# Kernel tuning notes

Measured on AMD Instinct MI355X. Metric: run time of the kernel, lower is better.

## Reference

```python
import jax, jax.numpy as jnp
import numpy as np

D = 128
NM = 1043
ND = 2166
EM = 300000
ED = 600000


def _gcn(x, src, dst, w, W, b):
    # symmetric-normalized weighted GCN conv: out = A_norm @ (x W^T) + b
    n = x.shape[0]
    deg = jax.ops.segment_sum(w, dst, num_segments=n)
    dinv = jnp.where(deg > 0, 1.0 / jnp.sqrt(deg), 0.0)
    norm = dinv[src] * w * dinv[dst]          # [E]
    h = x @ W.T                               # [n, D]
    return jax.ops.segment_sum(h[src] * norm[:, None], dst, num_segments=n) + b


def _encoder(x, edge, w, W1, b1, W2, b2):
    src, dst = edge[0], edge[1]
    x1 = jax.nn.relu(_gcn(x, src, dst, w, W1, b1))
    x2 = jax.nn.relu(_gcn(x1, src, dst, w, W2, b2))
    return x1, x2


def _layer_view_att(x, fc1_W, fc1_b, fc2_W, fc2_b):
    # x: [C, D, N]; channel attention over views/layers (LayerViewAttention)
    a = x.mean(axis=(1, 2))                            # global avg pool -> [C]
    a = jax.nn.relu(a @ fc1_W.T + fc1_b)
    a = jax.nn.sigmoid(a @ fc2_W.T + fc2_b)
    return jax.nn.relu(x * a[:, None, None])


def _fcn(x, W1, b1, W2, b2):
    # Fcn fusion: Linear -> ReLU -> Linear -> ReLU
    h = jax.nn.relu(x @ W1.T + b1)
    return jax.nn.relu(h @ W2.T + b2)


def setup_inputs():
    key = jax.random.key(0)
    ks = iter(jax.random.split(key, 64))

    def nrm(shape, s=0.05):
        return jax.random.normal(next(ks), shape, jnp.float32) * s

    inp = {}
    inp["mirna_x"] = jax.random.normal(next(ks), (NM, D), jnp.float32)
    inp["drug_x"] = jax.random.normal(next(ks), (ND, D), jnp.float32)
    for pre, n, e in [("m1", NM, EM), ("m2", NM, EM), ("d1", ND, ED), ("d2", ND, ED)]:
        inp[pre + "_edge"] = jax.random.randint(next(ks), (2, e), 0, n, jnp.int32)
        inp[pre + "_w"] = jax.random.uniform(next(ks), (e,), jnp.float32)
        inp[pre + "_W1"] = nrm((D, D))
        inp[pre + "_b1"] = jnp.zeros((D,), jnp.float32)
        inp[pre + "_W2"] = nrm((D, D))
        inp[pre + "_b2"] = jnp.zeros((D,), jnp.float32)
    inp["m_fc1_W"] = nrm((4, 4)); inp["m_fc1_b"] = jnp.zeros((4,), jnp.float32)
    inp["m_fc2_W"] = nrm((4, 4)); inp["m_fc2_b"] = jnp.zeros((4,), jnp.float32)
    inp["d_fc1_W"] = nrm((2, 2)); inp["d_fc1_b"] = jnp.zeros((2,), jnp.float32)
    inp["d_fc2_W"] = nrm((2, 2)); inp["d_fc2_b"] = jnp.zeros((2,), jnp.float32)
    inp["m_fus_W1"] = nrm((2 * D, 4 * D)); inp["m_fus_b1"] = jnp.zeros((2 * D,), jnp.float32)
    inp["m_fus_W2"] = nrm((D, 2 * D));     inp["m_fus_b2"] = jnp.zeros((D,), jnp.float32)
    inp["d_fus_W1"] = nrm((2 * D, 2 * D)); inp["d_fus_b1"] = jnp.zeros((2 * D,), jnp.float32)
    inp["d_fus_W2"] = nrm((D, 2 * D));     inp["d_fus_b2"] = jnp.zeros((D,), jnp.float32)
    return inp


def reference(mirna_x, drug_x,
              m1_edge, m1_w, m1_W1, m1_b1, m1_W2, m1_b2,
              m2_edge, m2_w, m2_W1, m2_b1, m2_W2, m2_b2,
              d1_edge, d1_w, d1_W1, d1_b1, d1_W2, d1_b2,
              d2_edge, d2_w, d2_W1, d2_b1, d2_W2, d2_b2,
              m_fc1_W, m_fc1_b, m_fc2_W, m_fc2_b,
              d_fc1_W, d_fc1_b, d_fc2_W, d_fc2_b,
              m_fus_W1, m_fus_b1, m_fus_W2, m_fus_b2,
              d_fus_W1, d_fus_b1, d_fus_W2, d_fus_b2):
    # miRNA: 2 views x 2 layers -> 4 channels
    m1a, m1b = _encoder(mirna_x, m1_edge, m1_w, m1_W1, m1_b1, m1_W2, m1_b2)
    m2a, m2b = _encoder(mirna_x, m2_edge, m2_w, m2_W1, m2_b1, m2_W2, m2_b2)
    mx = jnp.stack([m1a, m1b, m2a, m2b], axis=0).transpose(0, 2, 1)   # [4, D, NM]
    mx = _layer_view_att(mx, m_fc1_W, m_fc1_b, m_fc2_W, m_fc2_b)
    m_out = _fcn(mx.transpose(2, 0, 1).reshape(NM, 4 * D),
                 m_fus_W1, m_fus_b1, m_fus_W2, m_fus_b2)             # [NM, D]
    # drug: views summed per layer -> 2 channels
    d1a, d1b = _encoder(drug_x, d1_edge, d1_w, d1_W1, d1_b1, d1_W2, d1_b2)
    d2a, d2b = _encoder(drug_x, d2_edge, d2_w, d2_W1, d2_b1, d2_W2, d2_b2)
    dx = jnp.stack([d1a + d2a, d1b + d2b], axis=0).transpose(0, 2, 1)  # [2, D, ND]
    dx = _layer_view_att(dx, d_fc1_W, d_fc1_b, d_fc2_W, d_fc2_b)
    d_out = _fcn(dx.transpose(2, 0, 1).reshape(ND, 2 * D),
                 d_fus_W1, d_fus_b1, d_fus_W2, d_fus_b2)             # [ND, D]
    return jnp.concatenate([m_out, d_out], axis=0)                   # [NM+ND, D]
```

## Files before the change

kernel.cpp:

```cpp
#include <hip/hip_runtime.h>
#include <math.h>

#define D128 128
#define NM_ 1043
#define ND_ 2166
#define EM_ 300000
#define ED_ 600000
#define NBH 64
#define NMAX 2176
#define NTOT 6418
#define ETOT 1800000

struct ViewArgs {
    const int* edge[4];
    const float* w[4];
    int n[4], E[4];
    int cumn[5];
    int cumE[5];
    int rpo[4];
};

struct BiasArr { const float* b[4]; };

__global__ __launch_bounds__(1024) void hist_b(ViewArgs va, int* __restrict__ pcnt,
                                               float* __restrict__ pdeg) {
    __shared__ int lc[NMAX];
    __shared__ float ld[NMAX];
    const int view = blockIdx.x >> 6, vb = blockIdx.x & 63;
    const int n = va.n[view], E = va.E[view];
    const int* edge = va.edge[view];
    const float* w = va.w[view];
    for (int i = threadIdx.x; i < n; i += 1024) { lc[i] = 0; ld[i] = 0.f; }
    __syncthreads();
    const int per = (E + NBH - 1) / NBH;
    const int b = vb * per, e = min(E, b + per);
    for (int i = b + threadIdx.x; i < e; i += 1024) {
        int dst = edge[E + i];
        atomicAdd(&lc[dst], 1);
        atomicAdd(&ld[dst], w[i]);
    }
    __syncthreads();
    int* pc = pcnt + (size_t)NBH * va.cumn[view] + (size_t)vb * n;
    float* pd = pdeg + (size_t)NBH * va.cumn[view] + (size_t)vb * n;
    for (int i = threadIdx.x; i < n; i += 1024) { pc[i] = lc[i]; pd[i] = ld[i]; }
}

__global__ void colred_b(ViewArgs va, const int* __restrict__ pcnt,
                         const float* __restrict__ pdeg, int* __restrict__ cnt,
                         float* __restrict__ dinv) {
    int i = blockIdx.x * 256 + threadIdx.x;
    if (i >= NTOT) return;
    int view = 0;
    while (view < 3 && i >= va.cumn[view + 1]) ++view;
    const int il = i - va.cumn[view], n = va.n[view];
    const int* pc = pcnt + (size_t)NBH * va.cumn[view];
    const float* pd = pdeg + (size_t)NBH * va.cumn[view];
    int c = 0;
    float dg = 0.f;
    for (int b = 0; b < NBH; ++b) {
        c += pc[(size_t)b * n + il];
        dg += pd[(size_t)b * n + il];
    }
    cnt[i] = c;
    dinv[i] = dg > 0.f ? 1.0f / sqrtf(dg) : 0.f;
}

__global__ void scan_b(ViewArgs va, const int* __restrict__ cnt, int* __restrict__ rowptr) {
    __shared__ int wsum[4];
    const int view = blockIdx.x;
    const int n = va.n[view];
    const int* c = cnt + va.cumn[view];
    int* rp = rowptr + va.rpo[view];
    const int tid = threadIdx.x;
    const int per = (n + 255) / 256;
    const int b0 = tid * per, e0 = min(n, b0 + per);
    int s = 0;
    for (int i = b0; i < e0; ++i) s += c[i];
    const int lane = tid & 63, wid = tid >> 6;
    int sc = s;
    for (int off = 1; off < 64; off <<= 1) {
        int t = __shfl_up(sc, off);
        if (lane >= off) sc += t;
    }
    if (lane == 63) wsum[wid] = sc;
    __syncthreads();
    int wbase = 0;
    for (int wv = 0; wv < wid; ++wv) wbase += wsum[wv];
    int run = wbase + sc - s;
    if (tid == 0) rp[0] = 0;
    for (int i = b0; i < e0; ++i) {
        run += c[i];
        rp[i + 1] = run;
    }
}

__global__ void cum_b(ViewArgs va, const int* __restrict__ pcnt,
                      const int* __restrict__ rowptr, int* __restrict__ cum) {
    int i = blockIdx.x * 256 + threadIdx.x;
    if (i >= NTOT) return;
    int view = 0;
    while (view < 3 && i >= va.cumn[view + 1]) ++view;
    const int il = i - va.cumn[view], n = va.n[view];
    const int* pc = pcnt + (size_t)NBH * va.cumn[view];
    int* cm = cum + (size_t)NBH * va.cumn[view];
    int run = rowptr[va.rpo[view] + il];
    for (int b = 0; b < NBH; ++b) {
        cm[(size_t)b * n + il] = run;
        run += pc[(size_t)b * n + il];
    }
}

__global__ __launch_bounds__(1024) void fill2_b(ViewArgs va, const float* __restrict__ dinv,
                                                const int* __restrict__ cum,
                                                int2* __restrict__ spair) {
    __shared__ int lc[NMAX];
    const int view = blockIdx.x >> 6, vb = blockIdx.x & 63;
    const int n = va.n[view], E = va.E[view];
    const int* edge = va.edge[view];
    const float* w = va.w[view];
    const int* cm = cum + (size_t)NBH * va.cumn[view] + (size_t)vb * n;
    const float* dv = dinv + va.cumn[view];
    int2* sp = spair + va.cumE[view];
    for (int i = threadIdx.x; i < n; i += 1024) lc[i] = cm[i];
    __syncthreads();
    const int per = (E + NBH - 1) / NBH;
    const int b = vb * per, e = min(E, b + per);
    for (int i = b + threadIdx.x; i < e; i += 1024) {
        int src = edge[i];
        int dst = edge[E + i];
        int pos = atomicAdd(&lc[dst], 1);
        float nrm = dv[src] * w[i] * dv[dst];
        sp[pos] = make_int2(src, __float_as_int(nrm));
    }
}

__global__ __launch_bounds__(128) void agg_b(ViewArgs va, const int2* __restrict__ spair,
                                             const int* __restrict__ rowptr,
                                             const float* __restrict__ h, BiasArr ba,
                                             float* __restrict__ outbuf) {
    const int nf = blockIdx.x;
    int view = 0;
    while (view < 3 && nf >= va.cumn[view + 1]) ++view;
    const int ln = nf - va.cumn[view];
    const int* rp = rowptr + va.rpo[view];
    const int beg = rp[ln], end = rp[ln + 1];
    const int2* sp = spair + va.cumE[view];
    const float* hb = h + (size_t)va.cumn[view] * D128;
    const int tid = threadIdx.x;
    float a0 = 0.f, a1 = 0.f, a2 = 0.f, a3 = 0.f;
    int i = beg;
    for (; i + 4 <= end; i += 4) {
        int2 p0 = sp[i], p1 = sp[i + 1], p2 = sp[i + 2], p3 = sp[i + 3];
        a0 = fmaf(__int_as_float(p0.y), hb[(size_t)p0.x * D128 + tid], a0);
        a1 = fmaf(__int_as_float(p1.y), hb[(size_t)p1.x * D128 + tid], a1);
        a2 = fmaf(__int_as_float(p2.y), hb[(size_t)p2.x * D128 + tid], a2);
        a3 = fmaf(__int_as_float(p3.y), hb[(size_t)p3.x * D128 + tid], a3);
    }
    for (; i < end; ++i)
        a0 = fmaf(__int_as_float(sp[i].y), hb[(size_t)sp[i].x * D128 + tid], a0);
    float v = (a0 + a1) + (a2 + a3);
    outbuf[(size_t)nf * D128 + tid] = fmaxf(v + ba.b[view][tid], 0.f);
}

struct GSeg {
    const float* A;
    const float* W;
    const float* bias;
    float* C;
    int M, N, K, rowblks, blk0, relu;
};
struct GArgs { GSeg s[4]; int nseg; };

__global__ __launch_bounds__(256) void gemm_b(GArgs ga) {
    __shared__ float xs[32 * 64];
    __shared__ float wsm[128 * 64];
    int si = 0;
    while (si + 1 < ga.nseg && (int)blockIdx.x >= ga.s[si + 1].blk0) ++si;
    const GSeg S = ga.s[si];
    const int lb = blockIdx.x - S.blk0;
    const int rb = lb % S.rowblks, cb = lb / S.rowblks;
    const int row0 = rb * 32, col0 = cb * 128;
    const int tid = threadIdx.x;
    const int r0 = (tid >> 5) << 2;
    const int c0 = tid & 31;
    const int csw = (c0 & 7) << 2;
    float acc[4][4] = {};
    for (int kc = 0; kc < S.K; kc += 64) {
#pragma unroll
        for (int it = 0; it < 2; ++it) {
            int idx = tid + it * 256;
            int r = idx >> 4, k4 = (idx & 15) << 2;
            int gr = row0 + r;
            if (gr > S.M - 1) gr = S.M - 1;
            *(float4*)(xs + r * 64 + k4) =
                *(const float4*)(S.A + (size_t)gr * S.K + kc + k4);
        }
#pragma unroll
        for (int it = 0; it < 8; ++it) {
            int idx = tid + it * 256;
            int c = idx >> 4, k4 = (idx & 15) << 2;
            *(float4*)(wsm + c * 64 + (k4 ^ ((c & 7) << 2))) =
                *(const float4*)(S.W + (size_t)(col0 + c) * S.K + kc + k4);
        }
        __syncthreads();
#pragma unroll
        for (int k4 = 0; k4 < 64; k4 += 4) {
            float4 a0 = *(const float4*)(xs + (r0 + 0) * 64 + k4);
            float4 a1 = *(const float4*)(xs + (r0 + 1) * 64 + k4);
            float4 a2 = *(const float4*)(xs + (r0 + 2) * 64 + k4);
            float4 a3 = *(const float4*)(xs + (r0 + 3) * 64 + k4);
            const int sk = k4 ^ csw;
            float4 w0 = *(const float4*)(wsm + (c0 + 0) * 64 + sk);
            float4 w1 = *(const float4*)(wsm + (c0 + 32) * 64 + sk);
            float4 w2 = *(const float4*)(wsm + (c0 + 64) * 64 + sk);
            float4 w3 = *(const float4*)(wsm + (c0 + 96) * 64 + sk);
#define FMA4(i, av)                                                   \
            acc[i][0] = fmaf(av.x, w0.x, acc[i][0]); acc[i][0] = fmaf(av.y, w0.y, acc[i][0]); \
            acc[i][0] = fmaf(av.z, w0.z, acc[i][0]); acc[i][0] = fmaf(av.w, w0.w, acc[i][0]); \
            acc[i][1] = fmaf(av.x, w1.x, acc[i][1]); acc[i][1] = fmaf(av.y, w1.y, acc[i][1]); \
            acc[i][1] = fmaf(av.z, w1.z, acc[i][1]); acc[i][1] = fmaf(av.w, w1.w, acc[i][1]); \
            acc[i][2] = fmaf(av.x, w2.x, acc[i][2]); acc[i][2] = fmaf(av.y, w2.y, acc[i][2]); \
            acc[i][2] = fmaf(av.z, w2.z, acc[i][2]); acc[i][2] = fmaf(av.w, w2.w, acc[i][2]); \
            acc[i][3] = fmaf(av.x, w3.x, acc[i][3]); acc[i][3] = fmaf(av.y, w3.y, acc[i][3]); \
            acc[i][3] = fmaf(av.z, w3.z, acc[i][3]); acc[i][3] = fmaf(av.w, w3.w, acc[i][3]);
            FMA4(0, a0) FMA4(1, a1) FMA4(2, a2) FMA4(3, a3)
#undef FMA4
        }
        __syncthreads();
    }
#pragma unroll
    for (int i = 0; i < 4; ++i) {
        int gr = row0 + r0 + i;
        if (gr < S.M) {
#pragma unroll
            for (int j = 0; j < 4; ++j) {
                int gc = col0 + c0 + 32 * j;
                float v = acc[i][j];
                if (S.bias) v += S.bias[gc];
                if (S.relu) v = fmaxf(v, 0.f);
                S.C[(size_t)gr * S.N + gc] = v;
            }
        }
    }
}

struct SumArgs {
    const float* p[8];
    int cnt[8];
};

__global__ __launch_bounds__(256) void sum8_kernel(SumArgs args, float* __restrict__ sums) {
    __shared__ float red[256];
    const int ch = blockIdx.y;
    const float* x = args.p[ch];
    const int count = args.cnt[ch];
    float s = 0.f;
    for (int i = blockIdx.x * 256 + threadIdx.x; i < count; i += gridDim.x * 256) s += x[i];
    red[threadIdx.x] = s;
    __syncthreads();
    for (int off = 128; off > 0; off >>= 1) {
        if (threadIdx.x < off) red[threadIdx.x] += red[threadIdx.x + off];
        __syncthreads();
    }
    if (threadIdx.x == 0) atomicAdd(&sums[ch], red[0]);
}

__global__ void att_kernel(const float* __restrict__ sums,
                           const float* __restrict__ mW1, const float* __restrict__ mb1,
                           const float* __restrict__ mW2, const float* __restrict__ mb2,
                           const float* __restrict__ dW1, const float* __restrict__ db1,
                           const float* __restrict__ dW2, const float* __restrict__ db2,
                           float* __restrict__ scales) {
    if (threadIdx.x != 0 || blockIdx.x != 0) return;
    float mean[4], a[4];
    const float invM = 1.0f / (128.f * (float)NM_);
    for (int c = 0; c < 4; ++c) mean[c] = sums[c] * invM;
    for (int i = 0; i < 4; ++i) {
        float v = mb1[i];
        for (int j = 0; j < 4; ++j) v += mW1[i * 4 + j] * mean[j];
        a[i] = fmaxf(v, 0.f);
    }
    for (int c = 0; c < 4; ++c) {
        float v = mb2[c];
        for (int j = 0; j < 4; ++j) v += mW2[c * 4 + j] * a[j];
        scales[c] = 1.f / (1.f + expf(-v));
    }
    const float invD = 1.0f / (128.f * (float)ND_);
    float md[2] = {(sums[4] + sums[6]) * invD, (sums[5] + sums[7]) * invD};
    float ad[2];
    for (int i = 0; i < 2; ++i) {
        float v = db1[i];
        for (int j = 0; j < 2; ++j) v += dW1[i * 2 + j] * md[j];
        ad[i] = fmaxf(v, 0.f);
    }
    for (int c = 0; c < 2; ++c) {
        float v = db2[c];
        for (int j = 0; j < 2; ++j) v += dW2[c * 2 + j] * ad[j];
        scales[4 + c] = 1.f / (1.f + expf(-v));
    }
}

#define MCAT (NM_ * 512)
#define DCAT (ND_ * 256)

__global__ void cat_all(const float* __restrict__ l1, const float* __restrict__ l2,
                        const float* __restrict__ scales, float* __restrict__ catm,
                        float* __restrict__ catd) {
    int idx = blockIdx.x * 256 + threadIdx.x;
    if (idx < MCAT) {
        int i = idx >> 9;
        int k = idx & 511;
        int c = k >> 7;
        int j = k & 127;
        const float* p = (c == 0) ? l1 : (c == 1) ? l2
                         : (c == 2) ? l1 + (size_t)1043 * D128 : l2 + (size_t)1043 * D128;
        catm[idx] = fmaxf(scales[c] * p[(size_t)i * D128 + j], 0.f);
    } else if (idx < MCAT + DCAT) {
        int t = idx - MCAT;
        int i = t >> 8;
        int k = t & 255;
        int c = k >> 7;
        int j = k & 127;
        const float* pa = (c ? l2 : l1) + (size_t)2086 * D128;
        const float* pb = (c ? l2 : l1) + (size_t)4252 * D128;
        catd[t] = fmaxf(scales[4 + c] * (pa[(size_t)i * D128 + j] + pb[(size_t)i * D128 + j]), 0.f);
    }
}

extern "C" void kernel_launch(void* const* d_in, const int* in_sizes, int n_in,
                              void* d_out, int out_size, void* d_ws, size_t ws_size,
                              hipStream_t stream) {
    const float* mirna_x = (const float*)d_in[0];
    const float* drug_x  = (const float*)d_in[1];
    float* out = (float*)d_out;
    (void)in_sizes; (void)n_in; (void)out_size; (void)ws_size;

    char* ws = (char*)d_ws;
    auto AL = [](size_t x) { return (x + 255) & ~(size_t)255; };
    size_t o = 0;
    int2* spair = (int2*)(ws + o);   o += AL((size_t)ETOT * 8);
    int* cnt = (int*)(ws + o);       o += AL((size_t)NTOT * 4);
    int* rowptr = (int*)(ws + o);    o += AL((size_t)(NTOT + 4) * 4);
    float* dinv = (float*)(ws + o);  o += AL((size_t)NTOT * 4);
    float* sums = (float*)(ws + o);  o += 256;
    float* scales = (float*)(ws + o); o += 256;
    float* hbuf = (float*)(ws + o);  o += AL((size_t)NTOT * D128 * 4);
    float* l1out = (float*)(ws + o); o += AL((size_t)NTOT * D128 * 4);
    float* l2out = (float*)(ws + o); o += AL((size_t)NTOT * D128 * 4);
    const size_t R = o;
    int*   pcnt = (int*)(ws + R);
    float* pdeg = (float*)(ws + R + AL((size_t)NBH * NTOT * 4));
    int*   cum  = (int*)(ws + R + 2 * AL((size_t)NBH * NTOT * 4));
    float* catb_m = (float*)(ws + R);
    float* catb_d = (float*)(ws + R + AL((size_t)NM_ * 512 * 4));
    float* fush1_m = (float*)(ws + R + AL((size_t)NM_ * 512 * 4) + AL((size_t)ND_ * 256 * 4));
    float* fush1_d = fush1_m + (size_t)NM_ * 256;

    ViewArgs va;
    const int vb_in[4] = {2, 8, 14, 20};
    int nn[4] = {NM_, NM_, ND_, ND_};
    int ee[4] = {EM_, EM_, ED_, ED_};
    int cn = 0, ce = 0;
    for (int v = 0; v < 4; ++v) {
        va.edge[v] = (const int*)d_in[vb_in[v]];
        va.w[v] = (const float*)d_in[vb_in[v] + 1];
        va.n[v] = nn[v];
        va.E[v] = ee[v];
        va.cumn[v] = cn;
        va.cumE[v] = ce;
        va.rpo[v] = cn + v;
        cn += nn[v];
        ce += ee[v];
    }
    va.cumn[4] = cn;
    va.cumE[4] = ce;

    hipMemsetAsync(sums, 0, 8 * 4, stream);

    hist_b<<<256, 1024, 0, stream>>>(va, pcnt, pdeg);
    colred_b<<<(NTOT + 255) / 256, 256, 0, stream>>>(va, pcnt, pdeg, cnt, dinv);
    scan_b<<<4, 256, 0, stream>>>(va, cnt, rowptr);
    cum_b<<<(NTOT + 255) / 256, 256, 0, stream>>>(va, pcnt, rowptr, cum);
    fill2_b<<<256, 1024, 0, stream>>>(va, dinv, cum, spair);

    auto feat_gemm = [&](int layer, const float* l1src) {
        GArgs ga;
        ga.nseg = 4;
        int blk = 0;
        for (int v = 0; v < 4; ++v) {
            GSeg& S = ga.s[v];
            S.A = (layer == 1) ? ((v < 2) ? mirna_x : drug_x)
                               : l1src + (size_t)va.cumn[v] * D128;
            S.W = (const float*)d_in[vb_in[v] + (layer == 1 ? 2 : 4)];
            S.bias = nullptr;
            S.C = hbuf + (size_t)va.cumn[v] * D128;
            S.M = va.n[v]; S.N = 128; S.K = 128;
            S.rowblks = (va.n[v] + 31) / 32;
            S.blk0 = blk; S.relu = 0;
            blk += S.rowblks;
        }
        gemm_b<<<blk, 256, 0, stream>>>(ga);
    };
    BiasArr b1, b2;
    for (int v = 0; v < 4; ++v) {
        b1.b[v] = (const float*)d_in[vb_in[v] + 3];
        b2.b[v] = (const float*)d_in[vb_in[v] + 5];
    }

    feat_gemm(1, nullptr);
    agg_b<<<NTOT, 128, 0, stream>>>(va, spair, rowptr, hbuf, b1, l1out);
    feat_gemm(2, l1out);
    agg_b<<<NTOT, 128, 0, stream>>>(va, spair, rowptr, hbuf, b2, l2out);

    SumArgs sa;
    sa.p[0] = l1out;                      sa.p[1] = l2out;
    sa.p[2] = l1out + (size_t)1043 * 128; sa.p[3] = l2out + (size_t)1043 * 128;
    sa.p[4] = l1out + (size_t)2086 * 128; sa.p[5] = l2out + (size_t)2086 * 128;
    sa.p[6] = l1out + (size_t)4252 * 128; sa.p[7] = l2out + (size_t)4252 * 128;
    sa.cnt[0] = sa.cnt[1] = sa.cnt[2] = sa.cnt[3] = NM_ * D128;
    sa.cnt[4] = sa.cnt[5] = sa.cnt[6] = sa.cnt[7] = ND_ * D128;
    sum8_kernel<<<dim3(16, 8), 256, 0, stream>>>(sa, sums);
    att_kernel<<<1, 64, 0, stream>>>(sums,
        (const float*)d_in[26], (const float*)d_in[27], (const float*)d_in[28], (const float*)d_in[29],
        (const float*)d_in[30], (const float*)d_in[31], (const float*)d_in[32], (const float*)d_in[33],
        scales);

    cat_all<<<(MCAT + DCAT + 255) / 256, 256, 0, stream>>>(l1out, l2out, scales, catb_m, catb_d);

    {
        GArgs ga;
        ga.nseg = 2;
        ga.s[0] = {catb_m, (const float*)d_in[34], (const float*)d_in[35], fush1_m,
                   NM_, 256, 512, 33, 0, 1};
        ga.s[1] = {catb_d, (const float*)d_in[38], (const float*)d_in[39], fush1_d,
                   ND_, 256, 256, 68, 66, 1};
        gemm_b<<<66 + 136, 256, 0, stream>>>(ga);
    }
    {
        GArgs ga;
        ga.nseg = 2;
        ga.s[0] = {fush1_m, (const float*)d_in[36], (const float*)d_in[37], out,
                   NM_, 128, 256, 33, 0, 1};
        ga.s[1] = {fush1_d, (const float*)d_in[40], (const float*)d_in[41],
                   out + (size_t)NM_ * D128, ND_, 128, 256, 68, 33, 1};
        gemm_b<<<33 + 68, 256, 0, stream>>>(ga);
    }
}
```

Baseline: 273.6 us.

## Aggregate one node per wavefront with float2 gathers and XCD-aware block remap

The GCN aggregation kernel now assigns one destination node to each 64-lane wavefront (four nodes per 256-thread block) instead of a 128-thread block per node. Each lane gathers two features with float2 loads and reads the edge pairs two at a time as int4. Block indices are remapped so consecutive nodes land on the same XCD, which should improve L2 reuse of the gathered feature rows. The aim is fewer blocks, wider memory transactions and better cache locality for the memory-bound gather. The cost is extra alignment handling for odd row starts.

```diff
diff --git a/kernel.cpp b/kernel.cpp
--- a/kernel.cpp
+++ b/kernel.cpp
@@ -134,32 +134,69 @@
     }
 }
 
-__global__ __launch_bounds__(128) void agg_b(ViewArgs va, const int2* __restrict__ spair,
+#define AGG_BLKS ((NTOT + 3) / 4)
+
+__device__ __forceinline__ float2 fma2(float s, float2 h, float2 a) {
+    a.x = fmaf(s, h.x, a.x);
+    a.y = fmaf(s, h.y, a.y);
+    return a;
+}
+
+__global__ __launch_bounds__(256) void agg_b(ViewArgs va, const int2* __restrict__ spair,
                                              const int* __restrict__ rowptr,
                                              const float* __restrict__ h, BiasArr ba,
                                              float* __restrict__ outbuf) {
-    const int nf = blockIdx.x;
+    const int nblk = AGG_BLKS;
+    const int q = nblk >> 3, r = nblk & 7;
+    const int xcd = blockIdx.x & 7, idx = blockIdx.x >> 3;
+    const int bid = (xcd < r ? xcd * (q + 1) : r * (q + 1) + (xcd - r) * q) + idx;
+    const int wid = threadIdx.x >> 6, lane = threadIdx.x & 63;
+    const int nf = bid * 4 + wid;
+    if (nf >= NTOT) return;
     int view = 0;
     while (view < 3 && nf >= va.cumn[view + 1]) ++view;
     const int ln = nf - va.cumn[view];
     const int* rp = rowptr + va.rpo[view];
     const int beg = rp[ln], end = rp[ln + 1];
     const int2* sp = spair + va.cumE[view];
-    const float* hb = h + (size_t)va.cumn[view] * D128;
-    const int tid = threadIdx.x;
-    float a0 = 0.f, a1 = 0.f, a2 = 0.f, a3 = 0.f;
+    const float2* hb = (const float2*)(h + (size_t)va.cumn[view] * D128);
+    float2 a0 = {0.f, 0.f}, a1 = a0, a2 = a0, a3 = a0;
     int i = beg;
-    for (; i + 4 <= end; i += 4) {
-        int2 p0 = sp[i], p1 = sp[i + 1], p2 = sp[i + 2], p3 = sp[i + 3];
-        a0 = fmaf(__int_as_float(p0.y), hb[(size_t)p0.x * D128 + tid], a0);
-        a1 = fmaf(__int_as_float(p1.y), hb[(size_t)p1.x * D128 + tid], a1);
-        a2 = fmaf(__int_as_float(p2.y), hb[(size_t)p2.x * D128 + tid], a2);
-        a3 = fmaf(__int_as_float(p3.y), hb[(size_t)p3.x * D128 + tid], a3);
-    }
-    for (; i < end; ++i)
-        a0 = fmaf(__int_as_float(sp[i].y), hb[(size_t)sp[i].x * D128 + tid], a0);
-    float v = (a0 + a1) + (a2 + a3);
-    outbuf[(size_t)nf * D128 + tid] = fmaxf(v + ba.b[view][tid], 0.f);
+    if ((i & 1) && i < end) {
+        int2 p = sp[i];
+        a0 = fma2(__int_as_float(p.y), hb[(size_t)p.x * 64 + lane], a0);
+        ++i;
+    }
+    for (; i + 8 <= end; i += 8) {
+        int4 q0 = *(const int4*)(sp + i);
+        int4 q1 = *(const int4*)(sp + i + 2);
+        int4 q2 = *(const int4*)(sp + i + 4);
+        int4 q3 = *(const int4*)(sp + i + 6);
+        a0 = fma2(__int_as_float(q0.y), hb[(size_t)q0.x * 64 + lane], a0);
+        a1 = fma2(__int_as_float(q0.w), hb[(size_t)q0.z * 64 + lane], a1);
+        a2 = fma2(__int_as_float(q1.y), hb[(size_t)q1.x * 64 + lane], a2);
+        a3 = fma2(__int_as_float(q1.w), hb[(size_t)q1.z * 64 + lane], a3);
+        a0 = fma2(__int_as_float(q2.y), hb[(size_t)q2.x * 64 + lane], a0);
+        a1 = fma2(__int_as_float(q2.w), hb[(size_t)q2.z * 64 + lane], a1);
+        a2 = fma2(__int_as_float(q3.y), hb[(size_t)q3.x * 64 + lane], a2);
+        a3 = fma2(__int_as_float(q3.w), hb[(size_t)q3.z * 64 + lane], a3);
+    }
+    for (; i + 2 <= end; i += 2) {
+        int4 q0 = *(const int4*)(sp + i);
+        a0 = fma2(__int_as_float(q0.y), hb[(size_t)q0.x * 64 + lane], a0);
+        a1 = fma2(__int_as_float(q0.w), hb[(size_t)q0.z * 64 + lane], a1);
+    }
+    if (i < end) {
+        int2 p = sp[i];
+        a2 = fma2(__int_as_float(p.y), hb[(size_t)p.x * 64 + lane], a2);
+    }
+    float2 v;
+    v.x = (a0.x + a1.x) + (a2.x + a3.x);
+    v.y = (a0.y + a1.y) + (a2.y + a3.y);
+    float2 bb = *(const float2*)(ba.b[view] + lane * 2);
+    v.x = fmaxf(v.x + bb.x, 0.f);
+    v.y = fmaxf(v.y + bb.y, 0.f);
+    *(float2*)(outbuf + (size_t)nf * D128 + lane * 2) = v;
 }
 
 struct GSeg {
@@ -408,9 +445,9 @@
     }
 
     feat_gemm(1, nullptr);
-    agg_b<<<NTOT, 128, 0, stream>>>(va, spair, rowptr, hbuf, b1, l1out);
+    agg_b<<<AGG_BLKS, 256, 0, stream>>>(va, spair, rowptr, hbuf, b1, l1out);
     feat_gemm(2, l1out);
-    agg_b<<<NTOT, 128, 0, stream>>>(va, spair, rowptr, hbuf, b2, l2out);
+    agg_b<<<AGG_BLKS, 256, 0, stream>>>(va, spair, rowptr, hbuf, b2, l2out);
 
     SumArgs sa;
     sa.p[0] = l1out;                      sa.p[1] = l2out;
```

Measured after the change: 342.7 us. 25.3% more time.

## Fuse CSR metadata kernels, split aggregation edges across halves, fuse concat into GEMM

Applied to the files above, without the earlier changes.

Three separate kernels (column reduction, scan, cumulative offsets) are merged into one per-view kernel that keeps counts in shared memory. This removes two launches and the intermediate count buffer, but leaves only four blocks doing that work. The aggregation kernel now uses 256 threads per node, each 128-thread half summing half the edge list with an 8-way unroll, then combining through shared memory to raise memory-level parallelism. The scaled concat kernel is removed and its work is folded into the fusion GEMM's A-tile loads. This skips one full write and read of the concatenated buffer. The explicit ReLU is dropped there because the inputs are already non-negative.

```diff
diff --git a/kernel.cpp b/kernel.cpp
--- a/kernel.cpp
+++ b/kernel.cpp
@@ -45,37 +45,36 @@
     for (int i = threadIdx.x; i < n; i += 1024) { pc[i] = lc[i]; pd[i] = ld[i]; }
 }
 
-__global__ void colred_b(ViewArgs va, const int* __restrict__ pcnt,
-                         const float* __restrict__ pdeg, int* __restrict__ cnt,
-                         float* __restrict__ dinv) {
-    int i = blockIdx.x * 256 + threadIdx.x;
-    if (i >= NTOT) return;
-    int view = 0;
-    while (view < 3 && i >= va.cumn[view + 1]) ++view;
-    const int il = i - va.cumn[view], n = va.n[view];
+__global__ __launch_bounds__(1024) void csrmeta_b(ViewArgs va, const int* __restrict__ pcnt,
+                                                  const float* __restrict__ pdeg,
+                                                  float* __restrict__ dinv,
+                                                  int* __restrict__ rowptr,
+                                                  int* __restrict__ cum) {
+    __shared__ int lcnt[NMAX];
+    __shared__ int wsum[16];
+    const int view = blockIdx.x;
+    const int n = va.n[view];
     const int* pc = pcnt + (size_t)NBH * va.cumn[view];
     const float* pd = pdeg + (size_t)NBH * va.cumn[view];
-    int c = 0;
-    float dg = 0.f;
-    for (int b = 0; b < NBH; ++b) {
-        c += pc[(size_t)b * n + il];
-        dg += pd[(size_t)b * n + il];
-    }
-    cnt[i] = c;
-    dinv[i] = dg > 0.f ? 1.0f / sqrtf(dg) : 0.f;
-}
-
-__global__ void scan_b(ViewArgs va, const int* __restrict__ cnt, int* __restrict__ rowptr) {
-    __shared__ int wsum[4];
-    const int view = blockIdx.x;
-    const int n = va.n[view];
-    const int* c = cnt + va.cumn[view];
     int* rp = rowptr + va.rpo[view];
+    float* dv = dinv + va.cumn[view];
+    int* cm = cum + (size_t)NBH * va.cumn[view];
     const int tid = threadIdx.x;
-    const int per = (n + 255) / 256;
-    const int b0 = tid * per, e0 = min(n, b0 + per);
+    for (int i = tid; i < n; i += 1024) {
+        int c = 0;
+        float dg = 0.f;
+        for (int b = 0; b < NBH; ++b) {
+            c += pc[(size_t)b * n + i];
+            dg += pd[(size_t)b * n + i];
+        }
+        lcnt[i] = c;
+        dv[i] = dg > 0.f ? 1.0f / sqrtf(dg) : 0.f;
+    }
+    __syncthreads();
+    const int per = (n + 1023) / 1024;
+    const int b0 = min(n, tid * per), e0 = min(n, b0 + per);
     int s = 0;
-    for (int i = b0; i < e0; ++i) s += c[i];
+    for (int i = b0; i < e0; ++i) s += lcnt[i];
     const int lane = tid & 63, wid = tid >> 6;
     int sc = s;
     for (int off = 1; off < 64; off <<= 1) {
@@ -89,24 +88,18 @@
     int run = wbase + sc - s;
     if (tid == 0) rp[0] = 0;
     for (int i = b0; i < e0; ++i) {
-        run += c[i];
+        int c = lcnt[i];
+        lcnt[i] = run;
+        run += c;
         rp[i + 1] = run;
     }
-}
-
-__global__ void cum_b(ViewArgs va, const int* __restrict__ pcnt,
-                      const int* __restrict__ rowptr, int* __restrict__ cum) {
-    int i = blockIdx.x * 256 + threadIdx.x;
-    if (i >= NTOT) return;
-    int view = 0;
-    while (view < 3 && i >= va.cumn[view + 1]) ++view;
-    const int il = i - va.cumn[view], n = va.n[view];
-    const int* pc = pcnt + (size_t)NBH * va.cumn[view];
-    int* cm = cum + (size_t)NBH * va.cumn[view];
-    int run = rowptr[va.rpo[view] + il];
-    for (int b = 0; b < NBH; ++b) {
-        cm[(size_t)b * n + il] = run;
-        run += pc[(size_t)b * n + il];
+    __syncthreads();
+    for (int i = tid; i < n; i += 1024) {
+        int r = lcnt[i];
+        for (int b = 0; b < NBH; ++b) {
+            cm[(size_t)b * n + i] = r;
+            r += pc[(size_t)b * n + i];
+        }
     }
 }
 
@@ -134,10 +127,11 @@
     }
 }
 
-__global__ __launch_bounds__(128) void agg_b(ViewArgs va, const int2* __restrict__ spair,
+__global__ __launch_bounds__(256) void agg_b(ViewArgs va, const int2* __restrict__ spair,
                                              const int* __restrict__ rowptr,
                                              const float* __restrict__ h, BiasArr ba,
                                              float* __restrict__ outbuf) {
+    __shared__ float tmp[128];
     const int nf = blockIdx.x;
     int view = 0;
     while (view < 3 && nf >= va.cumn[view + 1]) ++view;
@@ -146,20 +140,34 @@
     const int beg = rp[ln], end = rp[ln + 1];
     const int2* sp = spair + va.cumE[view];
     const float* hb = h + (size_t)va.cumn[view] * D128;
-    const int tid = threadIdx.x;
+    const int col = threadIdx.x & 127;
+    const int half = threadIdx.x >> 7;
+    const int mid = beg + ((end - beg) >> 1);
+    int i = half ? mid : beg;
+    const int e = half ? end : mid;
     float a0 = 0.f, a1 = 0.f, a2 = 0.f, a3 = 0.f;
-    int i = beg;
-    for (; i + 4 <= end; i += 4) {
+    for (; i + 8 <= e; i += 8) {
         int2 p0 = sp[i], p1 = sp[i + 1], p2 = sp[i + 2], p3 = sp[i + 3];
-        a0 = fmaf(__int_as_float(p0.y), hb[(size_t)p0.x * D128 + tid], a0);
-        a1 = fmaf(__int_as_float(p1.y), hb[(size_t)p1.x * D128 + tid], a1);
-        a2 = fmaf(__int_as_float(p2.y), hb[(size_t)p2.x * D128 + tid], a2);
-        a3 = fmaf(__int_as_float(p3.y), hb[(size_t)p3.x * D128 + tid], a3);
-    }
-    for (; i < end; ++i)
-        a0 = fmaf(__int_as_float(sp[i].y), hb[(size_t)sp[i].x * D128 + tid], a0);
+        int2 p4 = sp[i + 4], p5 = sp[i + 5], p6 = sp[i + 6], p7 = sp[i + 7];
+        a0 = fmaf(__int_as_float(p0.y), hb[(size_t)p0.x * D128 + col], a0);
+        a1 = fmaf(__int_as_float(p1.y), hb[(size_t)p1.x * D128 + col], a1);
+        a2 = fmaf(__int_as_float(p2.y), hb[(size_t)p2.x * D128 + col], a2);
+        a3 = fmaf(__int_as_float(p3.y), hb[(size_t)p3.x * D128 + col], a3);
+        a0 = fmaf(__int_as_float(p4.y), hb[(size_t)p4.x * D128 + col], a0);
+        a1 = fmaf(__int_as_float(p5.y), hb[(size_t)p5.x * D128 + col], a1);
+        a2 = fmaf(__int_as_float(p6.y), hb[(size_t)p6.x * D128 + col], a2);
+        a3 = fmaf(__int_as_float(p7.y), hb[(size_t)p7.x * D128 + col], a3);
+    }
+    for (; i < e; ++i)
+        a0 = fmaf(__int_as_float(sp[i].y), hb[(size_t)sp[i].x * D128 + col], a0);
     float v = (a0 + a1) + (a2 + a3);
-    outbuf[(size_t)nf * D128 + tid] = fmaxf(v + ba.b[view][tid], 0.f);
+    if (half) tmp[col] = v;
+    __syncthreads();
+    if (!half) {
+        v += tmp[col];
+        v = fmaxf(v + ba.b[view][col], 0.f);
+        outbuf[(size_t)nf * D128 + col] = v;
+    }
 }
 
 struct GSeg {
@@ -167,9 +175,15 @@
     const float* W;
     const float* bias;
     float* C;
-    int M, N, K, rowblks, blk0, relu;
+    int M, N, K, rowblks, blk0, relu, mode;
 };
-struct GArgs { GSeg s[4]; int nseg; };
+struct GArgs {
+    GSeg s[4];
+    int nseg;
+    const float* l1;
+    const float* l2;
+    const float* scales;
+};
 
 __global__ __launch_bounds__(256) void gemm_b(GArgs ga) {
     __shared__ float xs[32 * 64];
@@ -192,8 +206,30 @@
             int r = idx >> 4, k4 = (idx & 15) << 2;
             int gr = row0 + r;
             if (gr > S.M - 1) gr = S.M - 1;
-            *(float4*)(xs + r * 64 + k4) =
-                *(const float4*)(S.A + (size_t)gr * S.K + kc + k4);
+            float4 v;
+            if (S.mode == 0) {
+                v = *(const float4*)(S.A + (size_t)gr * S.K + kc + k4);
+            } else {
+                int kk = kc + k4;
+                int c = kk >> 7, j = kk & 127;
+                if (S.mode == 1) {
+                    const float* base = (c == 0) ? ga.l1 : (c == 1) ? ga.l2
+                                       : (c == 2) ? ga.l1 + 133504 : ga.l2 + 133504;
+                    v = *(const float4*)(base + (size_t)gr * 128 + j);
+                    float s = ga.scales[c];
+                    v.x *= s; v.y *= s; v.z *= s; v.w *= s;
+                } else {
+                    const float* bp = c ? ga.l2 : ga.l1;
+                    float4 va4 = *(const float4*)(bp + 267008 + (size_t)gr * 128 + j);
+                    float4 vb4 = *(const float4*)(bp + 544256 + (size_t)gr * 128 + j);
+                    float s = ga.scales[4 + c];
+                    v.x = s * (va4.x + vb4.x);
+                    v.y = s * (va4.y + vb4.y);
+                    v.z = s * (va4.z + vb4.z);
+                    v.w = s * (va4.w + vb4.w);
+                }
+            }
+            *(float4*)(xs + r * 64 + k4) = v;
         }
 #pragma unroll
         for (int it = 0; it < 8; ++it) {
@@ -300,33 +336,6 @@
     }
 }
 
-#define MCAT (NM_ * 512)
-#define DCAT (ND_ * 256)
-
-__global__ void cat_all(const float* __restrict__ l1, const float* __restrict__ l2,
-                        const float* __restrict__ scales, float* __restrict__ catm,
-                        float* __restrict__ catd) {
-    int idx = blockIdx.x * 256 + threadIdx.x;
-    if (idx < MCAT) {
-        int i = idx >> 9;
-        int k = idx & 511;
-        int c = k >> 7;
-        int j = k & 127;
-        const float* p = (c == 0) ? l1 : (c == 1) ? l2
-                         : (c == 2) ? l1 + (size_t)1043 * D128 : l2 + (size_t)1043 * D128;
-        catm[idx] = fmaxf(scales[c] * p[(size_t)i * D128 + j], 0.f);
-    } else if (idx < MCAT + DCAT) {
-        int t = idx - MCAT;
-        int i = t >> 8;
-        int k = t & 255;
-        int c = k >> 7;
-        int j = k & 127;
-        const float* pa = (c ? l2 : l1) + (size_t)2086 * D128;
-        const float* pb = (c ? l2 : l1) + (size_t)4252 * D128;
-        catd[t] = fmaxf(scales[4 + c] * (pa[(size_t)i * D128 + j] + pb[(size_t)i * D128 + j]), 0.f);
-    }
-}
-
 extern "C" void kernel_launch(void* const* d_in, const int* in_sizes, int n_in,
                               void* d_out, int out_size, void* d_ws, size_t ws_size,
                               hipStream_t stream) {
@@ -339,7 +348,6 @@
     auto AL = [](size_t x) { return (x + 255) & ~(size_t)255; };
     size_t o = 0;
     int2* spair = (int2*)(ws + o);   o += AL((size_t)ETOT * 8);
-    int* cnt = (int*)(ws + o);       o += AL((size_t)NTOT * 4);
     int* rowptr = (int*)(ws + o);    o += AL((size_t)(NTOT + 4) * 4);
     float* dinv = (float*)(ws + o);  o += AL((size_t)NTOT * 4);
     float* sums = (float*)(ws + o);  o += 256;
@@ -348,12 +356,11 @@
     float* l1out = (float*)(ws + o); o += AL((size_t)NTOT * D128 * 4);
     float* l2out = (float*)(ws + o); o += AL((size_t)NTOT * D128 * 4);
     const size_t R = o;
+    const size_t psz = AL((size_t)NBH * NTOT * 4);
     int*   pcnt = (int*)(ws + R);
-    float* pdeg = (float*)(ws + R + AL((size_t)NBH * NTOT * 4));
-    int*   cum  = (int*)(ws + R + 2 * AL((size_t)NBH * NTOT * 4));
-    float* catb_m = (float*)(ws + R);
-    float* catb_d = (float*)(ws + R + AL((size_t)NM_ * 512 * 4));
-    float* fush1_m = (float*)(ws + R + AL((size_t)NM_ * 512 * 4) + AL((size_t)ND_ * 256 * 4));
+    float* pdeg = (float*)(ws + R + psz);
+    int*   cum  = (int*)(ws + R + 2 * psz);
+    float* fush1_m = (float*)(ws + R);
     float* fush1_d = fush1_m + (size_t)NM_ * 256;
 
     ViewArgs va;
@@ -378,14 +385,13 @@
     hipMemsetAsync(sums, 0, 8 * 4, stream);
 
     hist_b<<<256, 1024, 0, stream>>>(va, pcnt, pdeg);
-    colred_b<<<(NTOT + 255) / 256, 256, 0, stream>>>(va, pcnt, pdeg, cnt, dinv);
-    scan_b<<<4, 256, 0, stream>>>(va, cnt, rowptr);
-    cum_b<<<(NTOT + 255) / 256, 256, 0, stream>>>(va, pcnt, rowptr, cum);
+    csrmeta_b<<<4, 1024, 0, stream>>>(va, pcnt, pdeg, dinv, rowptr, cum);
     fill2_b<<<256, 1024, 0, stream>>>(va, dinv, cum, spair);
 
     auto feat_gemm = [&](int layer, const float* l1src) {
         GArgs ga;
         ga.nseg = 4;
+        ga.l1 = nullptr; ga.l2 = nullptr; ga.scales = nullptr;
         int blk = 0;
         for (int v = 0; v < 4; ++v) {
             GSeg& S = ga.s[v];
@@ -396,7 +402,7 @@
             S.C = hbuf + (size_t)va.cumn[v] * D128;
             S.M = va.n[v]; S.N = 128; S.K = 128;
             S.rowblks = (va.n[v] + 31) / 32;
-            S.blk0 = blk; S.relu = 0;
+            S.blk0 = blk; S.relu = 0; S.mode = 0;
             blk += S.rowblks;
         }
         gemm_b<<<blk, 256, 0, stream>>>(ga);
@@ -408,9 +414,9 @@
     }
 
     feat_gemm(1, nullptr);
-    agg_b<<<NTOT, 128, 0, stream>>>(va, spair, rowptr, hbuf, b1, l1out);
+    agg_b<<<NTOT, 256, 0, stream>>>(va, spair, rowptr, hbuf, b1, l1out);
     feat_gemm(2, l1out);
-    agg_b<<<NTOT, 128, 0, stream>>>(va, spair, rowptr, hbuf, b2, l2out);
+    agg_b<<<NTOT, 256, 0, stream>>>(va, spair, rowptr, hbuf, b2, l2out);
 
     SumArgs sa;
     sa.p[0] = l1out;                      sa.p[1] = l2out;
@@ -425,24 +431,24 @@
         (const float*)d_in[30], (const float*)d_in[31], (const float*)d_in[32], (const float*)d_in[33],
         scales);
 
-    cat_all<<<(MCAT + DCAT + 255) / 256, 256, 0, stream>>>(l1out, l2out, scales, catb_m, catb_d);
-
     {
         GArgs ga;
         ga.nseg = 2;
-        ga.s[0] = {catb_m, (const float*)d_in[34], (const float*)d_in[35], fush1_m,
-                   NM_, 256, 512, 33, 0, 1};
-        ga.s[1] = {catb_d, (const float*)d_in[38], (const float*)d_in[39], fush1_d,
-                   ND_, 256, 256, 68, 66, 1};
+        ga.l1 = l1out; ga.l2 = l2out; ga.scales = scales;
+        ga.s[0] = {nullptr, (const float*)d_in[34], (const float*)d_in[35], fush1_m,
+                   NM_, 256, 512, 33, 0, 1, 1};
+        ga.s[1] = {nullptr, (const float*)d_in[38], (const float*)d_in[39], fush1_d,
+                   ND_, 256, 256, 68, 66, 1, 2};
         gemm_b<<<66 + 136, 256, 0, stream>>>(ga);
     }
     {
         GArgs ga;
         ga.nseg = 2;
+        ga.l1 = nullptr; ga.l2 = nullptr; ga.scales = nullptr;
         ga.s[0] = {fush1_m, (const float*)d_in[36], (const float*)d_in[37], out,
-                   NM_, 128, 256, 33, 0, 1};
+                   NM_, 128, 256, 33, 0, 1, 0};
         ga.s[1] = {fush1_d, (const float*)d_in[40], (const float*)d_in[41],
-                   out + (size_t)NM_ * D128, ND_, 128, 256, 68, 33, 1};
+                   out + (size_t)NM_ * D128, ND_, 128, 256, 68, 33, 1, 0};
         gemm_b<<<33 + 68, 256, 0, stream>>>(ga);
     }
 }
```

New measurement: 346.3 us. 1.27x slower.
